# Kernel optimization log

Measured on AMD Instinct MI355X. Metric: run time of the kernel, lower is better.

The kernel has to match this reference:

```python
import jax, jax.numpy as jnp
import numpy as np

ALPHA = 0.8  # STE clipping threshold (unused in fwd-only path)


def binary_sign(x):
    # torch: x.sign() with zeros mapped to +1 => where(x >= 0, 1, -1)
    return jnp.where(x >= 0, jnp.ones((), x.dtype), -jnp.ones((), x.dtype))


def setup_inputs() -> dict:
    key = jax.random.key(0)
    ks = jax.random.split(key, 5)
    B, D = 16384, 4096
    x = jax.random.normal(ks[0], (B, D), dtype=jnp.float32)
    w0 = jax.random.normal(ks[1], (D, D), dtype=jnp.float32) * 0.1
    w1 = jax.random.normal(ks[2], (D, D), dtype=jnp.float32) * 0.1
    w2 = jax.random.normal(ks[3], (D, D), dtype=jnp.float32) * 0.1
    w3 = jax.random.normal(ks[4], (1, D), dtype=jnp.float32) * 0.1
    b0 = jnp.zeros((D,), jnp.float32)
    b1 = jnp.zeros((D,), jnp.float32)
    b2 = jnp.zeros((D,), jnp.float32)
    b3 = jnp.zeros((1,), jnp.float32)
    return {"x": x, "w0": w0, "b0": b0, "w1": w1, "b1": b1,
            "w2": w2, "b2": b2, "w3": w3, "b3": b3}


def reference(x, w0, b0, w1, b1, w2, b2, w3, b3):
    h = x
    for w, b in ((w0, b0), (w1, b1), (w2, b2), (w3, b3)):
        # BinaryLinear: binarize weights, dense matmul, add bias
        z = jnp.einsum('bi,oi->bo', h, binary_sign(w)) + b
        # BinaryActivation: binarize pre-activation
        h = binary_sign(z)
    return h  # [B, 1]
```

## Files before the change

kernel.cpp:

```cpp
#include <hip/hip_runtime.h>

typedef int   v4i  __attribute__((ext_vector_type(4)));
typedef int   v16i __attribute__((ext_vector_type(16)));
typedef float f4   __attribute__((ext_vector_type(4)));

#define DD 4096
#define BATCH 16384

__device__ __forceinline__ void gload16(const void* g, void* l) {
  __builtin_amdgcn_global_load_lds((const __attribute__((address_space(1))) void*)g,
                                   (__attribute__((address_space(3))) void*)l, 16, 0, 0);
}
#define ASM_VMCNT(n) asm volatile("s_waitcnt vmcnt(" #n ")" ::: "memory")
#define ASM_LGKM0()  asm volatile("s_waitcnt lgkmcnt(0)" ::: "memory")
#define BARF()       asm volatile("s_barrier" ::: "memory")

__device__ __forceinline__ int swz2(int row) { return ((row >> 1) & 3) ^ ((row >> 3) & 1); }

__global__ void binarize_swz_k(const float* __restrict__ w, unsigned char* __restrict__ o,
                               int swz_on) {
  int T = blockIdx.x * blockDim.x + threadIdx.x;
  int row = T >> 10, rem = T & 1023;
  int kblk = rem >> 4, seg = (rem >> 2) & 3, q = rem & 3;
  f4 v = *(const f4*)(w + (size_t)row * DD + kblk * 64 + seg * 16 + q * 4);
  unsigned int r = 0;
#pragma unroll
  for (int j = 0; j < 4; ++j) {
    unsigned int b = (v[j] >= 0.0f) ? 0x01u : 0xFFu;
    r |= b << (8 * j);
  }
  int slot = swz_on ? (seg ^ swz2(row)) : seg;
  *(unsigned int*)(o + (size_t)row * DD + kblk * 64 + slot * 16 + q * 4) = r;
}

__global__ void rowsum_k(const unsigned char* __restrict__ wb, int* __restrict__ R) {
  int lane = threadIdx.x & 63, wid = threadIdx.x >> 6;
  int row = blockIdx.x * 4 + wid;
  const unsigned char* p = wb + (size_t)row * DD;
  int s = 0;
#pragma unroll
  for (int j = 0; j < 4; ++j) {
    v4i a = *(const v4i*)(p + lane * 16 + j * 1024);
#pragma unroll
    for (int w = 0; w < 4; ++w) {
      unsigned int xa = (unsigned int)a[w];
#pragma unroll
      for (int by = 0; by < 4; ++by)
        s += (int)(signed char)((xa >> (8 * by)) & 255u);
    }
  }
#pragma unroll
  for (int off = 32; off > 0; off >>= 1) s += __shfl_down(s, off);
  if (lane == 0) R[row] = s;
}

__global__ void digitize_k(const float* __restrict__ x, unsigned char* __restrict__ Xd) {
  int T = blockIdx.x * blockDim.x + threadIdx.x;
  int row = T >> 10, rem = T & 1023;
  int kblk = rem >> 4, seg = (rem >> 2) & 3, q = rem & 3;
  f4 v = *(const f4*)(x + (size_t)row * DD + kblk * 64 + seg * 16 + q * 4);
  unsigned int Y[4];
#pragma unroll
  for (int j = 0; j < 4; ++j) {
    int X = (int)(v[j] * 134217728.0f);
    Y[j] = (unsigned int)(X + 1073741824);
  }
  size_t base = (size_t)row * 16384 + (size_t)kblk * 256;
  int r15 = row & 15;
#pragma unroll
  for (int d = 0; d < 4; ++d) {
    unsigned int wv = ((Y[0] >> (8 * d)) & 255u)
                    | (((Y[1] >> (8 * d)) & 255u) << 8)
                    | (((Y[2] >> (8 * d)) & 255u) << 16)
                    | (((Y[3] >> (8 * d)) & 255u) << 24);
    wv ^= 0x80808080u;
    int slot = ((d << 2) | seg) ^ r15;
    *(unsigned int*)(Xd + base + slot * 16 + q * 4) = wv;
  }
}

__global__ __launch_bounds__(256, 2) void gemm0p_k(
    const unsigned char* __restrict__ Xd, const unsigned char* __restrict__ wb,
    const int* __restrict__ R, const float* __restrict__ bias,
    signed char* __restrict__ h1) {
  __shared__ __align__(16) unsigned char As[2][64 * 256];
  __shared__ __align__(16) unsigned char Bs[2][128 * 64];
  const int tid = threadIdx.x, lane = tid & 63, wid = tid >> 6;
  const int wm = wid >> 1, wn = wid & 1;
  const int bid = blockIdx.x;
  const int xcd = bid & 7, sl = bid >> 3;
  const int m0 = ((xcd << 5) + (sl >> 5)) << 6;
  const int n0 = (sl & 31) << 7;

  v16i acc[4][2];
#pragma unroll
  for (int d = 0; d < 4; ++d)
#pragma unroll
    for (int f = 0; f < 2; ++f)
#pragma unroll
      for (int e = 0; e < 16; ++e) acc[d][f][e] = 0;

  auto stage = [&](int bf, int kb) {
#pragma unroll
    for (int i = 0; i < 4; ++i) {
      int c = wid * 4 + i;
      int lrow = c * 4 + (lane >> 4);
      const unsigned char* g = Xd + (size_t)(m0 + lrow) * 16384 + (size_t)kb * 256 + (lane & 15) * 16;
      gload16(g, &As[bf][c * 1024]);
    }
#pragma unroll
    for (int j = 0; j < 2; ++j) {
      int c = wid * 2 + j;
      int lrowB = c * 16 + (lane >> 2);
      const unsigned char* gB = wb + (size_t)(n0 + lrowB) * 4096 + kb * 64 + (lane & 3) * 16;
      gload16(gB, &Bs[bf][c * 1024]);
    }
  };

  const int rl = lane & 31, hi = lane >> 5;
  const int arow = wm * 32 + rl;
  const int r15 = arow & 15;

  stage(0, 0);
  stage(1, 1);
  ASM_VMCNT(6); BARF();
  int cur = 0;
  for (int t = 0; t < 64; ++t) {
    v4i af[2][4], bg[2][2];
#pragma unroll
    for (int kt = 0; kt < 2; ++kt) {
      int g = kt * 2 + hi;
#pragma unroll
      for (int d = 0; d < 4; ++d) {
        int slot = ((d << 2) | g) ^ r15;
        af[kt][d] = *(const v4i*)&As[cur][arow * 256 + slot * 16];
      }
#pragma unroll
      for (int f = 0; f < 2; ++f) {
        int brow = wn * 64 + f * 32 + rl;
        int slotb = g ^ swz2(brow);
        bg[kt][f] = *(const v4i*)&Bs[cur][brow * 64 + slotb * 16];
      }
    }
    ASM_LGKM0(); BARF();
    if (t < 62) stage(cur, t + 2);
    __builtin_amdgcn_s_setprio(1);
#pragma unroll
    for (int kt = 0; kt < 2; ++kt)
#pragma unroll
      for (int d = 0; d < 4; ++d)
#pragma unroll
        for (int f = 0; f < 2; ++f)
          acc[d][f] = __builtin_amdgcn_mfma_i32_32x32x32_i8(af[kt][d], bg[kt][f], acc[d][f], 0, 0, 0);
    __builtin_amdgcn_s_setprio(0);
    if (t < 62) { ASM_VMCNT(6); BARF(); }
    else if (t == 62) { ASM_VMCNT(0); BARF(); }
    cur ^= 1;
  }

#pragma unroll
  for (int f = 0; f < 2; ++f) {
    int col = n0 + wn * 64 + f * 32 + (lane & 31);
    long long rterm = 1082163328LL * (long long)R[col];
    double bb = (double)bias[col];
#pragma unroll
    for (int r = 0; r < 16; ++r) {
      long long Z = (long long)acc[0][f][r] + 256LL * (long long)acc[1][f][r]
                  + 65536LL * (long long)acc[2][f][r] + 16777216LL * (long long)acc[3][f][r]
                  + rterm;
      double z = (double)Z * 7.450580596923828125e-9 + bb;
      int row = m0 + wm * 32 + (r & 3) + 8 * (r >> 2) + 4 * (lane >> 5);
      int col2 = col ^ (swz2(row) << 4);
      h1[(size_t)row * DD + col2] = (z >= 0.0) ? (signed char)1 : (signed char)(-1);
    }
  }
}

__global__ __launch_bounds__(512, 2) void gemm0f_k(
    const float* __restrict__ x, const unsigned char* __restrict__ wb,
    const int* __restrict__ R, const float* __restrict__ bias,
    signed char* __restrict__ h1) {
  __shared__ signed char As[2][4][128 * 80];
  __shared__ signed char Bs[2][128 * 80];
  const int tid = threadIdx.x;
  const int lane = tid & 63, wid = tid >> 6;
  const int wm = wid >> 1, wn = wid & 1;
  const int n0 = blockIdx.x * 128, m0 = blockIdx.y * 128;

  v16i acc[4][2];
#pragma unroll
  for (int d = 0; d < 4; ++d)
#pragma unroll
    for (int f = 0; f < 2; ++f)
#pragma unroll
      for (int e = 0; e < 16; ++e) acc[d][f][e] = 0;

  const int arow_l = tid >> 4, aseg = tid & 15;
  const int brow = tid >> 2,  bseg = (tid & 3) * 16;
  f4 va[4]; v4i vb;

  auto loadTile = [&](int kpos) {
#pragma unroll
    for (int p = 0; p < 4; ++p)
      va[p] = *(const f4*)(x + (size_t)(m0 + p * 32 + arow_l) * DD + kpos + aseg * 4);
    vb = *(const v4i*)(wb + (size_t)(n0 + brow) * DD + kpos + bseg);
  };
  auto writeTile = [&](int bf) {
#pragma unroll
    for (int p = 0; p < 4; ++p) {
      int row = p * 32 + arow_l;
      unsigned int Y[4];
#pragma unroll
      for (int j = 0; j < 4; ++j) {
        int X = (int)(va[p][j] * 134217728.0f);
        Y[j] = (unsigned int)(X + 1073741824);
      }
#pragma unroll
      for (int k = 0; k < 4; ++k) {
        unsigned int wv = ((Y[0] >> (8 * k)) & 255u) | (((Y[1] >> (8 * k)) & 255u) << 8)
                        | (((Y[2] >> (8 * k)) & 255u) << 16) | (((Y[3] >> (8 * k)) & 255u) << 24);
        wv ^= 0x80808080u;
        *(unsigned int*)&As[bf][k][row * 80 + aseg * 4] = wv;
      }
    }
    *(v4i*)&Bs[bf][brow * 80 + bseg] = vb;
  };

  loadTile(0); writeTile(0);
  __syncthreads();
  for (int t = 0; t < 64; ++t) {
    int cur = t & 1;
    if (t < 63) loadTile((t + 1) * 64);
#pragma unroll
    for (int kt = 0; kt < 2; ++kt) {
      int g = kt * 2 + (lane >> 5);
      int ar = (wm * 32 + (lane & 31)) * 80 + g * 16;
      v4i a[4], b[2];
#pragma unroll
      for (int d = 0; d < 4; ++d) a[d] = *(const v4i*)&As[cur][d][ar];
#pragma unroll
      for (int f = 0; f < 2; ++f) {
        int br = wn * 64 + f * 32 + (lane & 31);
        int slotb = g ^ swz2(br);
        b[f] = *(const v4i*)&Bs[cur][br * 80 + slotb * 16];
      }
#pragma unroll
      for (int d = 0; d < 4; ++d)
#pragma unroll
        for (int f = 0; f < 2; ++f)
          acc[d][f] = __builtin_amdgcn_mfma_i32_32x32x32_i8(a[d], b[f], acc[d][f], 0, 0, 0);
    }
    if (t < 63) writeTile(cur ^ 1);
    __syncthreads();
  }

#pragma unroll
  for (int f = 0; f < 2; ++f) {
    int col = n0 + wn * 64 + f * 32 + (lane & 31);
    long long rterm = 1082163328LL * (long long)R[col];
    double bb = (double)bias[col];
#pragma unroll
    for (int r = 0; r < 16; ++r) {
      long long Z = (long long)acc[0][f][r] + 256LL * (long long)acc[1][f][r]
                  + 65536LL * (long long)acc[2][f][r] + 16777216LL * (long long)acc[3][f][r]
                  + rterm;
      double z = (double)Z * 7.450580596923828125e-9 + bb;
      int row = m0 + wm * 32 + (r & 3) + 8 * (r >> 2) + 4 * (lane >> 5);
      int col2 = col ^ (swz2(row) << 4);
      h1[(size_t)row * DD + col2] = (z >= 0.0) ? (signed char)1 : (signed char)(-1);
    }
  }
}

__global__ __launch_bounds__(256, 3) void gemm_bin_k(
    const unsigned char* __restrict__ A, const unsigned char* __restrict__ Bw,
    const float* __restrict__ bias, signed char* __restrict__ out) {
  __shared__ __align__(16) unsigned char As[2][128 * 64];
  __shared__ __align__(16) unsigned char Bs[2][128 * 64];
  const int tid = threadIdx.x, lane = tid & 63, wid = tid >> 6;
  const int wm = wid >> 1, wn = wid & 1;
  const int bid = blockIdx.x;
  const int xcd = bid & 7, sl = bid >> 3;
  const int m0 = ((xcd << 4) + (sl >> 5)) << 7;
  const int n0 = (sl & 31) << 7;

  v16i acc[2][2];
#pragma unroll
  for (int mi = 0; mi < 2; ++mi)
#pragma unroll
    for (int f = 0; f < 2; ++f)
#pragma unroll
      for (int e = 0; e < 16; ++e) acc[mi][f][e] = 0;

  auto stage = [&](int bf, int kb) {
#pragma unroll
    for (int j = 0; j < 2; ++j) {
      int c = wid * 2 + j;
      int lrow = c * 16 + (lane >> 2);
      const unsigned char* gA = A  + (size_t)(m0 + lrow) * 4096 + kb * 64 + (lane & 3) * 16;
      const unsigned char* gB = Bw + (size_t)(n0 + lrow) * 4096 + kb * 64 + (lane & 3) * 16;
      gload16(gA, &As[bf][c * 1024]);
      gload16(gB, &Bs[bf][c * 1024]);
    }
  };

  const int rl = lane & 31, hi = lane >> 5;

  stage(0, 0);
  stage(1, 1);
  ASM_VMCNT(4); BARF();
  int cur = 0;
  for (int t = 0; t < 64; ++t) {
    v4i af[2][2], bg[2][2];
#pragma unroll
    for (int kt = 0; kt < 2; ++kt) {
      int g = kt * 2 + hi;
#pragma unroll
      for (int mi = 0; mi < 2; ++mi) {
        int arow = wm * 64 + mi * 32 + rl;
        int slot = g ^ swz2(arow);
        af[kt][mi] = *(const v4i*)&As[cur][arow * 64 + slot * 16];
      }
#pragma unroll
      for (int f = 0; f < 2; ++f) {
        int brow = wn * 64 + f * 32 + rl;
        int slot = g ^ swz2(brow);
        bg[kt][f] = *(const v4i*)&Bs[cur][brow * 64 + slot * 16];
      }
    }
    ASM_LGKM0(); BARF();
    if (t < 62) stage(cur, t + 2);
    __builtin_amdgcn_s_setprio(1);
#pragma unroll
    for (int kt = 0; kt < 2; ++kt)
#pragma unroll
      for (int mi = 0; mi < 2; ++mi)
#pragma unroll
        for (int f = 0; f < 2; ++f)
          acc[mi][f] = __builtin_amdgcn_mfma_i32_32x32x32_i8(af[kt][mi], bg[kt][f], acc[mi][f], 0, 0, 0);
    __builtin_amdgcn_s_setprio(0);
    if (t < 62) { ASM_VMCNT(4); BARF(); }
    else if (t == 62) { ASM_VMCNT(0); BARF(); }
    cur ^= 1;
  }

#pragma unroll
  for (int mi = 0; mi < 2; ++mi)
#pragma unroll
    for (int f = 0; f < 2; ++f) {
      int col = n0 + wn * 64 + f * 32 + (lane & 31);
      float bb = bias[col];
#pragma unroll
      for (int r = 0; r < 16; ++r) {
        float z = (float)acc[mi][f][r] + bb;
        int row = m0 + wm * 64 + mi * 32 + (r & 3) + 8 * (r >> 2) + 4 * (lane >> 5);
        int col2 = col ^ (swz2(row) << 4);
        out[(size_t)row * DD + col2] = (z >= 0.0f) ? (signed char)1 : (signed char)(-1);
      }
    }
}

__global__ void final_k(const unsigned char* __restrict__ h, const unsigned char* __restrict__ w3b,
                        const float* __restrict__ b3, float* __restrict__ out) {
  int lane = threadIdx.x & 63, wid = threadIdx.x >> 6;
  int row = blockIdx.x * 4 + wid;
  int swz = swz2(row) << 4;
  const unsigned char* p = h + (size_t)row * DD;
  int s = 0;
#pragma unroll
  for (int j = 0; j < 4; ++j) {
    int e = lane * 16 + j * 1024;
    v4i a = *(const v4i*)(p + (e ^ swz));
    v4i b = *(const v4i*)(w3b + e);
#pragma unroll
    for (int w = 0; w < 4; ++w) {
      unsigned int xa = (unsigned int)a[w], xb = (unsigned int)b[w];
#pragma unroll
      for (int by = 0; by < 4; ++by)
        s += (int)(signed char)((xa >> (8 * by)) & 255u)
           * (int)(signed char)((xb >> (8 * by)) & 255u);
    }
  }
#pragma unroll
  for (int off = 32; off > 0; off >>= 1) s += __shfl_down(s, off);
  if (lane == 0) {
    float z = (float)s + b3[0];
    out[row] = (z >= 0.0f) ? 1.0f : -1.0f;
  }
}

extern "C" void kernel_launch(void* const* d_in, const int* in_sizes, int n_in,
                              void* d_out, int out_size, void* d_ws, size_t ws_size,
                              hipStream_t stream) {
  (void)in_sizes; (void)n_in; (void)out_size;
  const float* x  = (const float*)d_in[0];
  const float* w0 = (const float*)d_in[1];
  const float* b0 = (const float*)d_in[2];
  const float* w1 = (const float*)d_in[3];
  const float* b1 = (const float*)d_in[4];
  const float* w2 = (const float*)d_in[5];
  const float* b2 = (const float*)d_in[6];
  const float* w3 = (const float*)d_in[7];
  const float* b3 = (const float*)d_in[8];

  char* ws = (char*)d_ws;
  unsigned char* w0b = (unsigned char*)(ws + 0);
  unsigned char* w1b = (unsigned char*)(ws + (16ull << 20));
  unsigned char* w2b = (unsigned char*)(ws + (32ull << 20));
  unsigned char* w3b = (unsigned char*)(ws + (48ull << 20));
  int*           R   = (int*)(ws + (48ull << 20) + 65536);
  unsigned char* h1  = (unsigned char*)(ws + (64ull << 20));
  unsigned char* h2  = (unsigned char*)(ws + (128ull << 20));
  unsigned char* Xd  = (unsigned char*)(ws + (128ull << 20));
  float* out = (float*)d_out;

  binarize_swz_k<<<16384, 256, 0, stream>>>(w0, w0b, 1);
  binarize_swz_k<<<16384, 256, 0, stream>>>(w1, w1b, 1);
  binarize_swz_k<<<16384, 256, 0, stream>>>(w2, w2b, 1);
  binarize_swz_k<<<4,     256, 0, stream>>>(w3, w3b, 0);
  rowsum_k<<<1024, 256, 0, stream>>>(w0b, R);

  if (ws_size >= (384ull << 20)) {
    digitize_k<<<65536, 256, 0, stream>>>(x, Xd);
    gemm0p_k<<<8192, 256, 0, stream>>>(Xd, w0b, R, b0, (signed char*)h1);
  } else {
    gemm0f_k<<<dim3(32, 128), 512, 0, stream>>>(x, w0b, R, b0, (signed char*)h1);
  }
  gemm_bin_k<<<4096, 256, 0, stream>>>(h1, w1b, b1, (signed char*)h2);
  gemm_bin_k<<<4096, 256, 0, stream>>>(h2, w2b, b2, (signed char*)h1);
  final_k<<<4096, 256, 0, stream>>>(h1, w3b, b3, out);
}
```

Before: 1.891 ms.

## Load weight operand directly into registers, dropping its LDS staging

Both int8 GEMM kernels no longer stage the binarized weight tile through shared memory. Each wave now reads its B fragments straight from global memory into registers, prefetching one k-step ahead with two register buffers, and the vmcnt waits are adjusted to match. The aim is to cut LDS capacity use and the LDS write/read traffic for B. The cost is redundant global/L2 reads across waves sharing columns, strided 16-byte per-lane accesses, and global latency that only one iteration of prefetch has to hide.

Measured after the change: 2.382 ms. +26.0%, slower.

```diff
diff --git a/kernel.cpp b/kernel.cpp
--- a/kernel.cpp
+++ b/kernel.cpp
@@ -14,6 +14,7 @@
 #define ASM_VMCNT(n) asm volatile("s_waitcnt vmcnt(" #n ")" ::: "memory")
 #define ASM_LGKM0()  asm volatile("s_waitcnt lgkmcnt(0)" ::: "memory")
 #define BARF()       asm volatile("s_barrier" ::: "memory")
+#define SCHED0()     __builtin_amdgcn_sched_barrier(0)
 
 __device__ __forceinline__ int swz2(int row) { return ((row >> 1) & 3) ^ ((row >> 3) & 1); }
 
@@ -84,7 +85,6 @@
     const int* __restrict__ R, const float* __restrict__ bias,
     signed char* __restrict__ h1) {
   __shared__ __align__(16) unsigned char As[2][64 * 256];
-  __shared__ __align__(16) unsigned char Bs[2][128 * 64];
   const int tid = threadIdx.x, lane = tid & 63, wid = tid >> 6;
   const int wm = wid >> 1, wn = wid & 1;
   const int bid = blockIdx.x;
@@ -108,25 +108,29 @@
       const unsigned char* g = Xd + (size_t)(m0 + lrow) * 16384 + (size_t)kb * 256 + (lane & 15) * 16;
       gload16(g, &As[bf][c * 1024]);
     }
-#pragma unroll
-    for (int j = 0; j < 2; ++j) {
-      int c = wid * 2 + j;
-      int lrowB = c * 16 + (lane >> 2);
-      const unsigned char* gB = wb + (size_t)(n0 + lrowB) * 4096 + kb * 64 + (lane & 3) * 16;
-      gload16(gB, &Bs[bf][c * 1024]);
-    }
   };
 
   const int rl = lane & 31, hi = lane >> 5;
   const int arow = wm * 32 + rl;
   const int r15 = arow & 15;
 
-  stage(0, 0);
-  stage(1, 1);
-  ASM_VMCNT(6); BARF();
-  int cur = 0;
-  for (int t = 0; t < 64; ++t) {
-    v4i af[2][4], bg[2][2];
+  auto loadB = [&](v4i (&dst)[2][2], int kb) {
+#pragma unroll
+    for (int kt = 0; kt < 2; ++kt)
+#pragma unroll
+      for (int f = 0; f < 2; ++f) {
+        int brow = wn * 64 + f * 32 + rl;
+        int slot = (kt * 2 + hi) ^ swz2(brow);
+        dst[kt][f] = *(const v4i*)(wb + (size_t)(n0 + brow) * 4096 + kb * 64 + slot * 16);
+      }
+  };
+
+  v4i b0[2][2], b1[2][2];
+
+  auto body = [&](int t, int cur, v4i (&use)[2][2], v4i (&pre)[2][2]) {
+    if (t < 63) loadB(pre, t + 1);
+    SCHED0();
+    v4i af[2][4];
 #pragma unroll
     for (int kt = 0; kt < 2; ++kt) {
       int g = kt * 2 + hi;
@@ -135,12 +139,6 @@
         int slot = ((d << 2) | g) ^ r15;
         af[kt][d] = *(const v4i*)&As[cur][arow * 256 + slot * 16];
       }
-#pragma unroll
-      for (int f = 0; f < 2; ++f) {
-        int brow = wn * 64 + f * 32 + rl;
-        int slotb = g ^ swz2(brow);
-        bg[kt][f] = *(const v4i*)&Bs[cur][brow * 64 + slotb * 16];
-      }
     }
     ASM_LGKM0(); BARF();
     if (t < 62) stage(cur, t + 2);
@@ -151,11 +149,19 @@
       for (int d = 0; d < 4; ++d)
 #pragma unroll
         for (int f = 0; f < 2; ++f)
-          acc[d][f] = __builtin_amdgcn_mfma_i32_32x32x32_i8(af[kt][d], bg[kt][f], acc[d][f], 0, 0, 0);
+          acc[d][f] = __builtin_amdgcn_mfma_i32_32x32x32_i8(af[kt][d], use[kt][f], acc[d][f], 0, 0, 0);
     __builtin_amdgcn_s_setprio(0);
-    if (t < 62) { ASM_VMCNT(6); BARF(); }
+    if (t < 62) { ASM_VMCNT(4); BARF(); }
     else if (t == 62) { ASM_VMCNT(0); BARF(); }
-    cur ^= 1;
+  };
+
+  stage(0, 0);
+  stage(1, 1);
+  loadB(b0, 0);
+  ASM_VMCNT(0); BARF();
+  for (int t2 = 0; t2 < 64; t2 += 2) {
+    body(t2,     (t2 >> 1) & 1 ? 0 : 0, b0, b1);
+    body(t2 + 1, 1, b1, b0);
   }
 
 #pragma unroll
@@ -276,7 +282,6 @@
     const unsigned char* __restrict__ A, const unsigned char* __restrict__ Bw,
     const float* __restrict__ bias, signed char* __restrict__ out) {
   __shared__ __align__(16) unsigned char As[2][128 * 64];
-  __shared__ __align__(16) unsigned char Bs[2][128 * 64];
   const int tid = threadIdx.x, lane = tid & 63, wid = tid >> 6;
   const int wm = wid >> 1, wn = wid & 1;
   const int bid = blockIdx.x;
@@ -297,35 +302,37 @@
     for (int j = 0; j < 2; ++j) {
       int c = wid * 2 + j;
       int lrow = c * 16 + (lane >> 2);
-      const unsigned char* gA = A  + (size_t)(m0 + lrow) * 4096 + kb * 64 + (lane & 3) * 16;
-      const unsigned char* gB = Bw + (size_t)(n0 + lrow) * 4096 + kb * 64 + (lane & 3) * 16;
+      const unsigned char* gA = A + (size_t)(m0 + lrow) * 4096 + kb * 64 + (lane & 3) * 16;
       gload16(gA, &As[bf][c * 1024]);
-      gload16(gB, &Bs[bf][c * 1024]);
     }
   };
 
   const int rl = lane & 31, hi = lane >> 5;
 
-  stage(0, 0);
-  stage(1, 1);
-  ASM_VMCNT(4); BARF();
-  int cur = 0;
-  for (int t = 0; t < 64; ++t) {
-    v4i af[2][2], bg[2][2];
+  auto loadB = [&](v4i (&dst)[2][2], int kb) {
+#pragma unroll
+    for (int kt = 0; kt < 2; ++kt)
+#pragma unroll
+      for (int f = 0; f < 2; ++f) {
+        int brow = wn * 64 + f * 32 + rl;
+        int slot = (kt * 2 + hi) ^ swz2(brow);
+        dst[kt][f] = *(const v4i*)(Bw + (size_t)(n0 + brow) * 4096 + kb * 64 + slot * 16);
+      }
+  };
+
+  v4i b0[2][2], b1[2][2];
+
+  auto body = [&](int t, int cur, v4i (&use)[2][2], v4i (&pre)[2][2]) {
+    if (t < 63) loadB(pre, t + 1);
+    SCHED0();
+    v4i af[2][2];
 #pragma unroll
     for (int kt = 0; kt < 2; ++kt) {
       int g = kt * 2 + hi;
 #pragma unroll
       for (int mi = 0; mi < 2; ++mi) {
         int arow = wm * 64 + mi * 32 + rl;
-        int slot = g ^ swz2(arow);
-        af[kt][mi] = *(const v4i*)&As[cur][arow * 64 + slot * 16];
-      }
-#pragma unroll
-      for (int f = 0; f < 2; ++f) {
-        int brow = wn * 64 + f * 32 + rl;
-        int slot = g ^ swz2(brow);
-        bg[kt][f] = *(const v4i*)&Bs[cur][brow * 64 + slot * 16];
+        af[kt][mi] = *(const v4i*)&As[cur][arow * 64 + ((g ^ swz2(arow)) * 16)];
       }
     }
     ASM_LGKM0(); BARF();
@@ -337,11 +344,19 @@
       for (int mi = 0; mi < 2; ++mi)
 #pragma unroll
         for (int f = 0; f < 2; ++f)
-          acc[mi][f] = __builtin_amdgcn_mfma_i32_32x32x32_i8(af[kt][mi], bg[kt][f], acc[mi][f], 0, 0, 0);
+          acc[mi][f] = __builtin_amdgcn_mfma_i32_32x32x32_i8(af[kt][mi], use[kt][f], acc[mi][f], 0, 0, 0);
     __builtin_amdgcn_s_setprio(0);
-    if (t < 62) { ASM_VMCNT(4); BARF(); }
+    if (t < 62) { ASM_VMCNT(2); BARF(); }
     else if (t == 62) { ASM_VMCNT(0); BARF(); }
-    cur ^= 1;
+  };
+
+  stage(0, 0);
+  stage(1, 1);
+  loadB(b0, 0);
+  ASM_VMCNT(0); BARF();
+  for (int t2 = 0; t2 < 64; t2 += 2) {
+    body(t2,     0, b0, b1);
+    body(t2 + 1, 1, b1, b0);
   }
 
 #pragma unroll
```

## Triple-buffer LDS and interleave fragment reads, staging and MFMA in GEMM loops

Applied to the files above, without the earlier changes.

Both int8 GEMM kernels move from double to triple LDS buffering. The next-next tile is now staged into the third buffer, which removes the mid-iteration barrier between the LDS reads and the global-to-LDS loads. The K-loop is split into sub-steps that interleave ds_reads, split global_load_lds issues and MFMA groups, using partial lgkmcnt waits and sched_barrier fences. The goal is to hide LDS latency behind MFMAs and drop one barrier per iteration. The cost is more LDS per block, which could lower occupancy at the requested launch bounds, and the setprio hints are removed.

New measurement: 2.326 ms. +23.0%, slower.

```diff
diff --git a/kernel.cpp b/kernel.cpp
--- a/kernel.cpp
+++ b/kernel.cpp
@@ -12,8 +12,9 @@
                                    (__attribute__((address_space(3))) void*)l, 16, 0, 0);
 }
 #define ASM_VMCNT(n) asm volatile("s_waitcnt vmcnt(" #n ")" ::: "memory")
-#define ASM_LGKM0()  asm volatile("s_waitcnt lgkmcnt(0)" ::: "memory")
+#define ASM_LGKM(n)  asm volatile("s_waitcnt lgkmcnt(" #n ")" ::: "memory")
 #define BARF()       asm volatile("s_barrier" ::: "memory")
+#define SCHED0()     __builtin_amdgcn_sched_barrier(0)
 
 __device__ __forceinline__ int swz2(int row) { return ((row >> 1) & 3) ^ ((row >> 3) & 1); }
 
@@ -83,8 +84,8 @@
     const unsigned char* __restrict__ Xd, const unsigned char* __restrict__ wb,
     const int* __restrict__ R, const float* __restrict__ bias,
     signed char* __restrict__ h1) {
-  __shared__ __align__(16) unsigned char As[2][64 * 256];
-  __shared__ __align__(16) unsigned char Bs[2][128 * 64];
+  __shared__ __align__(16) unsigned char As[3][64 * 256];
+  __shared__ __align__(16) unsigned char Bs[3][128 * 64];
   const int tid = threadIdx.x, lane = tid & 63, wid = tid >> 6;
   const int wm = wid >> 1, wn = wid & 1;
   const int bid = blockIdx.x;
@@ -100,62 +101,88 @@
 #pragma unroll
       for (int e = 0; e < 16; ++e) acc[d][f][e] = 0;
 
-  auto stage = [&](int bf, int kb) {
-#pragma unroll
-    for (int i = 0; i < 4; ++i) {
-      int c = wid * 4 + i;
+  auto stageA2 = [&](int bf, int kb, int half) {
+#pragma unroll
+    for (int i = 0; i < 2; ++i) {
+      int c = wid * 4 + half * 2 + i;
       int lrow = c * 4 + (lane >> 4);
       const unsigned char* g = Xd + (size_t)(m0 + lrow) * 16384 + (size_t)kb * 256 + (lane & 15) * 16;
       gload16(g, &As[bf][c * 1024]);
     }
-#pragma unroll
-    for (int j = 0; j < 2; ++j) {
-      int c = wid * 2 + j;
-      int lrowB = c * 16 + (lane >> 2);
-      const unsigned char* gB = wb + (size_t)(n0 + lrowB) * 4096 + kb * 64 + (lane & 3) * 16;
-      gload16(gB, &Bs[bf][c * 1024]);
-    }
+  };
+  auto stageB1 = [&](int bf, int kb, int half) {
+    int c = wid * 2 + half;
+    int lrowB = c * 16 + (lane >> 2);
+    const unsigned char* gB = wb + (size_t)(n0 + lrowB) * 4096 + kb * 64 + (lane & 3) * 16;
+    gload16(gB, &Bs[bf][c * 1024]);
   };
 
   const int rl = lane & 31, hi = lane >> 5;
   const int arow = wm * 32 + rl;
   const int r15 = arow & 15;
-
-  stage(0, 0);
-  stage(1, 1);
+  const int brow0 = wn * 64 + rl;
+  const int brow1 = wn * 64 + 32 + rl;
+  const int bsw0 = swz2(brow0), bsw1 = swz2(brow1);
+
+  auto readA2 = [&](v4i* dst, int bf, int dh, int ks) {
+    int g = ks * 2 + hi;
+#pragma unroll
+    for (int j = 0; j < 2; ++j) {
+      int d = 2 * dh + j;
+      int slot = ((d << 2) | g) ^ r15;
+      dst[j] = *(const v4i*)&As[bf][arow * 256 + slot * 16];
+    }
+  };
+  auto readB2 = [&](v4i* dst, int bf, int ks) {
+    int g = ks * 2 + hi;
+    dst[0] = *(const v4i*)&Bs[bf][brow0 * 64 + ((g ^ bsw0) * 16)];
+    dst[1] = *(const v4i*)&Bs[bf][brow1 * 64 + ((g ^ bsw1) * 16)];
+  };
+
+  stageA2(0, 0, 0); stageA2(0, 0, 1); stageB1(0, 0, 0); stageB1(0, 0, 1);
+  stageA2(1, 1, 0); stageA2(1, 1, 1); stageB1(1, 1, 0); stageB1(1, 1, 1);
   ASM_VMCNT(6); BARF();
-  int cur = 0;
-  for (int t = 0; t < 64; ++t) {
-    v4i af[2][4], bg[2][2];
-#pragma unroll
-    for (int kt = 0; kt < 2; ++kt) {
-      int g = kt * 2 + hi;
-#pragma unroll
-      for (int d = 0; d < 4; ++d) {
-        int slot = ((d << 2) | g) ^ r15;
-        af[kt][d] = *(const v4i*)&As[cur][arow * 256 + slot * 16];
-      }
-#pragma unroll
-      for (int f = 0; f < 2; ++f) {
-        int brow = wn * 64 + f * 32 + rl;
-        int slotb = g ^ swz2(brow);
-        bg[kt][f] = *(const v4i*)&Bs[cur][brow * 64 + slotb * 16];
-      }
-    }
-    ASM_LGKM0(); BARF();
-    if (t < 62) stage(cur, t + 2);
-    __builtin_amdgcn_s_setprio(1);
-#pragma unroll
-    for (int kt = 0; kt < 2; ++kt)
-#pragma unroll
-      for (int d = 0; d < 4; ++d)
-#pragma unroll
-        for (int f = 0; f < 2; ++f)
-          acc[d][f] = __builtin_amdgcn_mfma_i32_32x32x32_i8(af[kt][d], bg[kt][f], acc[d][f], 0, 0, 0);
-    __builtin_amdgcn_s_setprio(0);
-    if (t < 62) { ASM_VMCNT(6); BARF(); }
-    else if (t == 62) { ASM_VMCNT(0); BARF(); }
-    cur ^= 1;
+
+  int p = 0;
+  v4i aA[2], aB[2], aC[2], aD[2], bK0[2], bK1[2];
+  for (int kb = 0; kb < 64; ++kb) {
+    const int s = (p >= 1) ? p - 1 : 2;
+    const bool st = (kb < 62);
+    readA2(aA, p, 0, 0); readB2(bK0, p, 0);
+    readA2(aB, p, 1, 0);
+    if (st) stageA2(s, kb + 2, 0);
+    ASM_LGKM(2); SCHED0();
+#pragma unroll
+    for (int j = 0; j < 2; ++j)
+#pragma unroll
+      for (int f = 0; f < 2; ++f)
+        acc[j][f] = __builtin_amdgcn_mfma_i32_32x32x32_i8(aA[j], bK0[f], acc[j][f], 0, 0, 0);
+    readA2(aC, p, 0, 1); readB2(bK1, p, 1);
+    if (st) stageA2(s, kb + 2, 1);
+    ASM_LGKM(4); SCHED0();
+#pragma unroll
+    for (int j = 0; j < 2; ++j)
+#pragma unroll
+      for (int f = 0; f < 2; ++f)
+        acc[2 + j][f] = __builtin_amdgcn_mfma_i32_32x32x32_i8(aB[j], bK0[f], acc[2 + j][f], 0, 0, 0);
+    readA2(aD, p, 1, 1);
+    if (st) stageB1(s, kb + 2, 0);
+    ASM_LGKM(2); SCHED0();
+#pragma unroll
+    for (int j = 0; j < 2; ++j)
+#pragma unroll
+      for (int f = 0; f < 2; ++f)
+        acc[j][f] = __builtin_amdgcn_mfma_i32_32x32x32_i8(aC[j], bK1[f], acc[j][f], 0, 0, 0);
+    if (st) stageB1(s, kb + 2, 1);
+    ASM_LGKM(0); SCHED0();
+#pragma unroll
+    for (int j = 0; j < 2; ++j)
+#pragma unroll
+      for (int f = 0; f < 2; ++f)
+        acc[2 + j][f] = __builtin_amdgcn_mfma_i32_32x32x32_i8(aD[j], bK1[f], acc[2 + j][f], 0, 0, 0);
+    if (kb < 62)      { ASM_VMCNT(6); BARF(); }
+    else if (kb == 62){ ASM_VMCNT(0); BARF(); }
+    p = (p < 2) ? p + 1 : 0;
   }
 
 #pragma unroll
@@ -275,8 +302,8 @@
 __global__ __launch_bounds__(256, 3) void gemm_bin_k(
     const unsigned char* __restrict__ A, const unsigned char* __restrict__ Bw,
     const float* __restrict__ bias, signed char* __restrict__ out) {
-  __shared__ __align__(16) unsigned char As[2][128 * 64];
-  __shared__ __align__(16) unsigned char Bs[2][128 * 64];
+  __shared__ __align__(16) unsigned char As[3][128 * 64];
+  __shared__ __align__(16) unsigned char Bs[3][128 * 64];
   const int tid = threadIdx.x, lane = tid & 63, wid = tid >> 6;
   const int wm = wid >> 1, wn = wid & 1;
   const int bid = blockIdx.x;
@@ -292,56 +319,67 @@
 #pragma unroll
       for (int e = 0; e < 16; ++e) acc[mi][f][e] = 0;
 
-  auto stage = [&](int bf, int kb) {
+  auto stageA = [&](int bf, int kb) {
 #pragma unroll
     for (int j = 0; j < 2; ++j) {
       int c = wid * 2 + j;
       int lrow = c * 16 + (lane >> 2);
-      const unsigned char* gA = A  + (size_t)(m0 + lrow) * 4096 + kb * 64 + (lane & 3) * 16;
+      const unsigned char* gA = A + (size_t)(m0 + lrow) * 4096 + kb * 64 + (lane & 3) * 16;
+      gload16(gA, &As[bf][c * 1024]);
+    }
+  };
+  auto stageB = [&](int bf, int kb) {
+#pragma unroll
+    for (int j = 0; j < 2; ++j) {
+      int c = wid * 2 + j;
+      int lrow = c * 16 + (lane >> 2);
       const unsigned char* gB = Bw + (size_t)(n0 + lrow) * 4096 + kb * 64 + (lane & 3) * 16;
-      gload16(gA, &As[bf][c * 1024]);
       gload16(gB, &Bs[bf][c * 1024]);
     }
   };
 
   const int rl = lane & 31, hi = lane >> 5;
-
-  stage(0, 0);
-  stage(1, 1);
+  const int arow0 = wm * 64 + rl,      arow1 = wm * 64 + 32 + rl;
+  const int brow0 = wn * 64 + rl,      brow1 = wn * 64 + 32 + rl;
+  const int asw0 = swz2(arow0), asw1 = swz2(arow1);
+  const int bsw0 = swz2(brow0), bsw1 = swz2(brow1);
+
+  auto readKS = [&](v4i* fa, v4i* fb, int bf, int ks) {
+    int g = ks * 2 + hi;
+    fa[0] = *(const v4i*)&As[bf][arow0 * 64 + ((g ^ asw0) * 16)];
+    fa[1] = *(const v4i*)&As[bf][arow1 * 64 + ((g ^ asw1) * 16)];
+    fb[0] = *(const v4i*)&Bs[bf][brow0 * 64 + ((g ^ bsw0) * 16)];
+    fb[1] = *(const v4i*)&Bs[bf][brow1 * 64 + ((g ^ bsw1) * 16)];
+  };
+
+  stageA(0, 0); stageB(0, 0);
+  stageA(1, 1); stageB(1, 1);
   ASM_VMCNT(4); BARF();
-  int cur = 0;
-  for (int t = 0; t < 64; ++t) {
-    v4i af[2][2], bg[2][2];
-#pragma unroll
-    for (int kt = 0; kt < 2; ++kt) {
-      int g = kt * 2 + hi;
-#pragma unroll
-      for (int mi = 0; mi < 2; ++mi) {
-        int arow = wm * 64 + mi * 32 + rl;
-        int slot = g ^ swz2(arow);
-        af[kt][mi] = *(const v4i*)&As[cur][arow * 64 + slot * 16];
-      }
-#pragma unroll
-      for (int f = 0; f < 2; ++f) {
-        int brow = wn * 64 + f * 32 + rl;
-        int slot = g ^ swz2(brow);
-        bg[kt][f] = *(const v4i*)&Bs[cur][brow * 64 + slot * 16];
-      }
-    }
-    ASM_LGKM0(); BARF();
-    if (t < 62) stage(cur, t + 2);
-    __builtin_amdgcn_s_setprio(1);
-#pragma unroll
-    for (int kt = 0; kt < 2; ++kt)
-#pragma unroll
-      for (int mi = 0; mi < 2; ++mi)
-#pragma unroll
-        for (int f = 0; f < 2; ++f)
-          acc[mi][f] = __builtin_amdgcn_mfma_i32_32x32x32_i8(af[kt][mi], bg[kt][f], acc[mi][f], 0, 0, 0);
-    __builtin_amdgcn_s_setprio(0);
-    if (t < 62) { ASM_VMCNT(4); BARF(); }
-    else if (t == 62) { ASM_VMCNT(0); BARF(); }
-    cur ^= 1;
+
+  int p = 0;
+  v4i fa0[2], fb0[2], fa1[2], fb1[2];
+  for (int kb = 0; kb < 64; ++kb) {
+    const int s = (p >= 1) ? p - 1 : 2;
+    const bool st = (kb < 62);
+    readKS(fa0, fb0, p, 0);
+    readKS(fa1, fb1, p, 1);
+    if (st) stageA(s, kb + 2);
+    ASM_LGKM(4); SCHED0();
+#pragma unroll
+    for (int mi = 0; mi < 2; ++mi)
+#pragma unroll
+      for (int f = 0; f < 2; ++f)
+        acc[mi][f] = __builtin_amdgcn_mfma_i32_32x32x32_i8(fa0[mi], fb0[f], acc[mi][f], 0, 0, 0);
+    if (st) stageB(s, kb + 2);
+    ASM_LGKM(0); SCHED0();
+#pragma unroll
+    for (int mi = 0; mi < 2; ++mi)
+#pragma unroll
+      for (int f = 0; f < 2; ++f)
+        acc[mi][f] = __builtin_amdgcn_mfma_i32_32x32x32_i8(fa1[mi], fb1[f], acc[mi][f], 0, 0, 0);
+    if (kb < 62)      { ASM_VMCNT(4); BARF(); }
+    else if (kb == 62){ ASM_VMCNT(0); BARF(); }
+    p = (p < 2) ? p + 1 : 0;
   }
 
 #pragma unroll
```

## Use 3-byte digitized input for first GEMM with exact fixup of near-zero outputs

Applied to the files above, without the earlier changes.

Quantizes x to 24-bit fixed point split into three int8 planes instead of four, so the first layer needs 3/4 of the int8 MFMAs and reads less A data. Outputs whose pre-activation lies close to zero are appended to a worklist through an atomic counter. A separate fixup kernel recomputes those entries at full 32-bit fixed-point precision so their signs match the original path. This adds a small kernel, atomic traffic and a capped worklist; entries beyond the cap would not be corrected.

After: 1.772 ms, median of 2. -6.3%, faster.

```diff
diff --git a/kernel.cpp b/kernel.cpp
--- a/kernel.cpp
+++ b/kernel.cpp
@@ -6,6 +6,7 @@
 
 #define DD 4096
 #define BATCH 16384
+#define FIXCAP (1u << 22)
 
 __device__ __forceinline__ void gload16(const void* g, void* l) {
   __builtin_amdgcn_global_load_lds((const __attribute__((address_space(1))) void*)g,
@@ -54,7 +55,7 @@
   if (lane == 0) R[row] = s;
 }
 
-__global__ void digitize_k(const float* __restrict__ x, unsigned char* __restrict__ Xd) {
+__global__ void digitize3_k(const float* __restrict__ x, unsigned char* __restrict__ Xp) {
   int T = blockIdx.x * blockDim.x + threadIdx.x;
   int row = T >> 10, rem = T & 1023;
   int kblk = rem >> 4, seg = (rem >> 2) & 3, q = rem & 3;
@@ -62,28 +63,30 @@
   unsigned int Y[4];
 #pragma unroll
   for (int j = 0; j < 4; ++j) {
-    int X = (int)(v[j] * 134217728.0f);
-    Y[j] = (unsigned int)(X + 1073741824);
-  }
-  size_t base = (size_t)row * 16384 + (size_t)kblk * 256;
-  int r15 = row & 15;
-#pragma unroll
-  for (int d = 0; d < 4; ++d) {
+    int X = (int)(v[j] * 524288.0f);
+    Y[j] = (unsigned int)(X + 8388608);
+  }
+  int slot = seg ^ swz2(row);
+  size_t base = (size_t)row * DD + kblk * 64 + slot * 16 + q * 4;
+#pragma unroll
+  for (int d = 0; d < 3; ++d) {
     unsigned int wv = ((Y[0] >> (8 * d)) & 255u)
                     | (((Y[1] >> (8 * d)) & 255u) << 8)
                     | (((Y[2] >> (8 * d)) & 255u) << 16)
                     | (((Y[3] >> (8 * d)) & 255u) << 24);
     wv ^= 0x80808080u;
-    int slot = ((d << 2) | seg) ^ r15;
-    *(unsigned int*)(Xd + base + slot * 16 + q * 4) = wv;
-  }
-}
-
-__global__ __launch_bounds__(256, 2) void gemm0p_k(
-    const unsigned char* __restrict__ Xd, const unsigned char* __restrict__ wb,
+    *(unsigned int*)(Xp + (size_t)d * (64u << 20) + base) = wv;
+  }
+}
+
+__global__ void zeroc_k(unsigned int* c) { if (threadIdx.x == 0) *c = 0; }
+
+__global__ __launch_bounds__(256, 2) void gemm0p3_k(
+    const unsigned char* __restrict__ Xp, const unsigned char* __restrict__ wb,
     const int* __restrict__ R, const float* __restrict__ bias,
-    signed char* __restrict__ h1) {
-  __shared__ __align__(16) unsigned char As[2][64 * 256];
+    signed char* __restrict__ h1,
+    unsigned int* __restrict__ wl, unsigned int* __restrict__ cnt) {
+  __shared__ __align__(16) unsigned char Asp[2][3][64 * 64];
   __shared__ __align__(16) unsigned char Bs[2][128 * 64];
   const int tid = threadIdx.x, lane = tid & 63, wid = tid >> 6;
   const int wm = wid >> 1, wn = wid & 1;
@@ -92,9 +95,9 @@
   const int m0 = ((xcd << 5) + (sl >> 5)) << 6;
   const int n0 = (sl & 31) << 7;
 
-  v16i acc[4][2];
-#pragma unroll
-  for (int d = 0; d < 4; ++d)
+  v16i acc[3][2];
+#pragma unroll
+  for (int d = 0; d < 3; ++d)
 #pragma unroll
     for (int f = 0; f < 2; ++f)
 #pragma unroll
@@ -102,11 +105,13 @@
 
   auto stage = [&](int bf, int kb) {
 #pragma unroll
-    for (int i = 0; i < 4; ++i) {
-      int c = wid * 4 + i;
-      int lrow = c * 4 + (lane >> 4);
-      const unsigned char* g = Xd + (size_t)(m0 + lrow) * 16384 + (size_t)kb * 256 + (lane & 15) * 16;
-      gload16(g, &As[bf][c * 1024]);
+    for (int i = 0; i < 3; ++i) {
+      int c = wid * 3 + i;
+      int d = c >> 2, sub = c & 3;
+      int lrow = sub * 16 + (lane >> 2);
+      const unsigned char* g = Xp + (size_t)d * (64u << 20)
+                             + (size_t)(m0 + lrow) * 4096 + kb * 64 + (lane & 3) * 16;
+      gload16(g, &Asp[bf][d][sub * 1024]);
     }
 #pragma unroll
     for (int j = 0; j < 2; ++j) {
@@ -119,28 +124,24 @@
 
   const int rl = lane & 31, hi = lane >> 5;
   const int arow = wm * 32 + rl;
-  const int r15 = arow & 15;
+  const int asw = swz2(arow);
+  const int brow0 = wn * 64 + rl, brow1 = wn * 64 + 32 + rl;
+  const int bsw0 = swz2(brow0), bsw1 = swz2(brow1);
 
   stage(0, 0);
   stage(1, 1);
-  ASM_VMCNT(6); BARF();
+  ASM_VMCNT(5); BARF();
   int cur = 0;
   for (int t = 0; t < 64; ++t) {
-    v4i af[2][4], bg[2][2];
+    v4i af[2][3], bg[2][2];
 #pragma unroll
     for (int kt = 0; kt < 2; ++kt) {
       int g = kt * 2 + hi;
 #pragma unroll
-      for (int d = 0; d < 4; ++d) {
-        int slot = ((d << 2) | g) ^ r15;
-        af[kt][d] = *(const v4i*)&As[cur][arow * 256 + slot * 16];
-      }
-#pragma unroll
-      for (int f = 0; f < 2; ++f) {
-        int brow = wn * 64 + f * 32 + rl;
-        int slotb = g ^ swz2(brow);
-        bg[kt][f] = *(const v4i*)&Bs[cur][brow * 64 + slotb * 16];
-      }
+      for (int d = 0; d < 3; ++d)
+        af[kt][d] = *(const v4i*)&Asp[cur][d][arow * 64 + ((g ^ asw) * 16)];
+      bg[kt][0] = *(const v4i*)&Bs[cur][brow0 * 64 + ((g ^ bsw0) * 16)];
+      bg[kt][1] = *(const v4i*)&Bs[cur][brow1 * 64 + ((g ^ bsw1) * 16)];
     }
     ASM_LGKM0(); BARF();
     if (t < 62) stage(cur, t + 2);
@@ -148,12 +149,12 @@
 #pragma unroll
     for (int kt = 0; kt < 2; ++kt)
 #pragma unroll
-      for (int d = 0; d < 4; ++d)
+      for (int d = 0; d < 3; ++d)
 #pragma unroll
         for (int f = 0; f < 2; ++f)
           acc[d][f] = __builtin_amdgcn_mfma_i32_32x32x32_i8(af[kt][d], bg[kt][f], acc[d][f], 0, 0, 0);
     __builtin_amdgcn_s_setprio(0);
-    if (t < 62) { ASM_VMCNT(6); BARF(); }
+    if (t < 62) { ASM_VMCNT(5); BARF(); }
     else if (t == 62) { ASM_VMCNT(0); BARF(); }
     cur ^= 1;
   }
@@ -161,15 +162,50 @@
 #pragma unroll
   for (int f = 0; f < 2; ++f) {
     int col = n0 + wn * 64 + f * 32 + (lane & 31);
-    long long rterm = 1082163328LL * (long long)R[col];
+    long long rterm = 32896LL * (long long)R[col];
     double bb = (double)bias[col];
 #pragma unroll
     for (int r = 0; r < 16; ++r) {
       long long Z = (long long)acc[0][f][r] + 256LL * (long long)acc[1][f][r]
-                  + 65536LL * (long long)acc[2][f][r] + 16777216LL * (long long)acc[3][f][r]
-                  + rterm;
-      double z = (double)Z * 7.450580596923828125e-9 + bb;
+                  + 65536LL * (long long)acc[2][f][r] + rterm;
+      double z = (double)Z * 1.9073486328125e-6 + bb;
       int row = m0 + wm * 32 + (r & 3) + 8 * (r >> 2) + 4 * (lane >> 5);
+      int col2 = col ^ (swz2(row) << 4);
+      h1[(size_t)row * DD + col2] = (z >= 0.0) ? (signed char)1 : (signed char)(-1);
+      if (fabs(z) <= 0.0079) {
+        unsigned int idx = atomicAdd(cnt, 1u);
+        if (idx < FIXCAP) wl[idx] = ((unsigned int)row << 12) | (unsigned int)col;
+      }
+    }
+  }
+}
+
+__global__ void fixup_k(const float* __restrict__ x, const unsigned char* __restrict__ wb,
+                        const float* __restrict__ bias, const unsigned int* __restrict__ wl,
+                        const unsigned int* __restrict__ cnt, signed char* __restrict__ h1) {
+  unsigned int n = *cnt; if (n > FIXCAP) n = FIXCAP;
+  int lane = threadIdx.x & 63;
+  int gw = (blockIdx.x * blockDim.x + threadIdx.x) >> 6;
+  int nw = (gridDim.x * blockDim.x) >> 6;
+  for (unsigned int e = gw; e < n; e += nw) {
+    unsigned int ent = wl[e];
+    int row = ent >> 12, col = ent & 4095;
+    const float* xr = x + (size_t)row * DD;
+    const unsigned char* wr = wb + (size_t)col * DD;
+    int sw = swz2(col);
+    long long s = 0;
+#pragma unroll 4
+    for (int j = 0; j < 64; ++j) {
+      int k = j * 64 + lane;
+      int kk = (k & ~63) + ((((k >> 4) & 3) ^ sw) * 16) + (k & 15);
+      signed char w = (signed char)wr[kk];
+      long long X = (long long)(int)(xr[k] * 134217728.0f);
+      s += (w > 0) ? X : -X;
+    }
+#pragma unroll
+    for (int off = 32; off > 0; off >>= 1) s += __shfl_down(s, off);
+    if (lane == 0) {
+      double z = (double)s * 7.450580596923828125e-9 + (double)bias[col];
       int col2 = col ^ (swz2(row) << 4);
       h1[(size_t)row * DD + col2] = (z >= 0.0) ? (signed char)1 : (signed char)(-1);
     }
@@ -411,7 +447,9 @@
   int*           R   = (int*)(ws + (48ull << 20) + 65536);
   unsigned char* h1  = (unsigned char*)(ws + (64ull << 20));
   unsigned char* h2  = (unsigned char*)(ws + (128ull << 20));
-  unsigned char* Xd  = (unsigned char*)(ws + (128ull << 20));
+  unsigned char* Xp  = (unsigned char*)(ws + (128ull << 20));
+  unsigned int*  cnt = (unsigned int*)(ws + (320ull << 20));
+  unsigned int*  wl  = (unsigned int*)(ws + (320ull << 20) + 64);
   float* out = (float*)d_out;
 
   binarize_swz_k<<<16384, 256, 0, stream>>>(w0, w0b, 1);
@@ -421,8 +459,10 @@
   rowsum_k<<<1024, 256, 0, stream>>>(w0b, R);
 
   if (ws_size >= (384ull << 20)) {
-    digitize_k<<<65536, 256, 0, stream>>>(x, Xd);
-    gemm0p_k<<<8192, 256, 0, stream>>>(Xd, w0b, R, b0, (signed char*)h1);
+    digitize3_k<<<65536, 256, 0, stream>>>(x, Xp);
+    zeroc_k<<<1, 64, 0, stream>>>(cnt);
+    gemm0p3_k<<<8192, 256, 0, stream>>>(Xp, w0b, R, b0, (signed char*)h1, wl, cnt);
+    fixup_k<<<2048, 256, 0, stream>>>(x, w0b, b0, wl, cnt, (signed char*)h1);
   } else {
     gemm0f_k<<<dim3(32, 128), 512, 0, stream>>>(x, w0b, R, b0, (signed char*)h1);
   }
```
